# Kernel tuning notes

Hardware: AMD Instinct MI355X
Metric: run time of the kernel (lower is better)

## Reference

```python
import jax, jax.numpy as jnp
import numpy as np

B, C, H, W = 2, 128, 64, 256
G, P, EXP = 8, 4, 2
D = C // G


def _conv1x1(x, w, b):
    # x: (b,c,h,w), w: (o,c), b: (o,)
    return jnp.einsum('bchw,oc->bohw', x, w) + b[None, :, None, None]


def _lin_sample(value, x):
    # value: (b,g,d,h,w); x: (b,g,p,h,w) pixel coords along W -> (b,g,d,p,h,w)
    Bv, Gv, Dv, Hv, Wv = value.shape
    Pv = x.shape[2]
    xc = jnp.clip(x, 0.0, Wv - 1.0)
    x0 = jnp.floor(xc)
    i0 = x0.astype(jnp.int32)
    i1 = jnp.minimum(i0 + 1, Wv - 1)
    t = (xc - x0)[:, :, None]  # (b,g,1,p,h,w)
    shape = (Bv, Gv, Dv, Pv, Hv, Wv)
    v = jnp.broadcast_to(value[:, :, :, None], shape)
    v0 = jnp.take_along_axis(v, jnp.broadcast_to(i0[:, :, None], shape), axis=-1)
    v1 = jnp.take_along_axis(v, jnp.broadcast_to(i1[:, :, None], shape), axis=-1)
    return v0 * (1.0 - t) + v1 * t


def _layernorm_c(x, g, b):
    mu = jnp.mean(x, axis=1, keepdims=True)
    var = jnp.mean((x - mu) ** 2, axis=1, keepdims=True)
    return (x - mu) * jax.lax.rsqrt(var + 1e-5) * g[None, :, None, None] + b[None, :, None, None]


def _forward(ml, mr, fl, fr, nl, nr, gml, gmr, cap, gap,
             wv, bv, wn, bn, woc, boc, wog, bog, wa, ba, wo, bo,
             lw, lb, w1, b1, w2, b2):
    mask = jnp.concatenate([gml, gmr], axis=0)   # (2B,1,H,W)
    q = jnp.concatenate([ml, mr], axis=0)        # (2B,C,H,W)
    ctx = jnp.concatenate([fr, fl], axis=0)      # cross: right feats for left queries
    geo = jnp.concatenate([nr, nl], axis=0)      # (2B,3,H,W)
    B2 = q.shape[0]
    # deformable 1D cross-attention (normal-guided)
    value = _conv1x1(ctx, wv, bv).reshape(B2, G, D, H, W)
    nfeat = _conv1x1(geo, wn, bn).reshape(B2, G, D, H, W)
    off_c = _conv1x1(q, woc, boc).reshape(B2, G, P, H, W)
    off_g = _conv1x1(q, wog, bog).reshape(B2, G, P, H, W)
    attn = jax.nn.softmax(_conv1x1(q, wa, ba).reshape(B2, G, 2 * P, H, W), axis=2)
    ctx_kp = jnp.clip(cap * (W - 1.0) + off_c, 0.0, W - 1.0)
    geo_kp = jnp.clip(gap * (W - 1.0) + off_g, 0.0, W - 1.0)
    s_ctx = _lin_sample(value, ctx_kp)           # (2B,G,D,P,H,W)
    s_geo = _lin_sample(nfeat, geo_kp)
    sampled = jnp.concatenate([s_ctx, s_geo], axis=3)  # (2B,G,D,2P,H,W)
    agg = jnp.einsum('bgdphw,bgphw->bgdhw', sampled, attn).reshape(B2, C, H, W)
    upd = _conv1x1(agg, wo, bo) * mask
    # residual + LayerNorm over channels + 1x1-conv FFN
    x = q + upd
    x = _layernorm_c(x, lw, lb)
    h1 = _conv1x1(x, w1, b1)
    x = x + _conv1x1(h1 * jax.nn.sigmoid(h1), w2, b2)
    return x, ctx_kp, geo_kp


def setup_inputs() -> dict:
    key = jax.random.key(0)
    ks = jax.random.split(key, 20)
    f32 = jnp.float32
    def n(k, shape, s=1.0):
        return jax.random.normal(k, shape, dtype=f32) * s
    return {
        'match_left': n(ks[0], (B, C, H, W)),
        'match_right': n(ks[1], (B, C, H, W)),
        'feat_left': n(ks[2], (B, C, H, W)),
        'feat_right': n(ks[3], (B, C, H, W)),
        'normal_left': n(ks[4], (B, 3, H, W)),
        'normal_right': n(ks[5], (B, 3, H, W)),
        'gate_mask_left': jax.random.uniform(ks[6], (B, 1, H, W), dtype=f32),
        'gate_mask_right': jax.random.uniform(ks[7], (B, 1, H, W), dtype=f32),
        'context_anchor_points': jax.random.uniform(ks[8], (2 * B, G, P, H, W), dtype=f32),
        'geometric_anchor_points': jax.random.uniform(ks[9], (2 * B, G, P, H, W), dtype=f32),
        'w_value': n(ks[10], (C, C), 0.02), 'b_value': jnp.zeros((C,), f32),
        'w_normal': n(ks[11], (C, 3), 0.02), 'b_normal': jnp.zeros((C,), f32),
        'w_off_ctx': n(ks[12], (G * P, C), 0.02), 'b_off_ctx': jnp.zeros((G * P,), f32),
        'w_off_geo': n(ks[13], (G * P, C), 0.02), 'b_off_geo': jnp.zeros((G * P,), f32),
        'w_attn': n(ks[14], (G * 2 * P, C), 0.02), 'b_attn': jnp.zeros((G * 2 * P,), f32),
        'w_out': n(ks[15], (C, C), 0.02), 'b_out': jnp.zeros((C,), f32),
        'ln_w': jnp.ones((C,), f32), 'ln_b': jnp.zeros((C,), f32),
        'w_ff1': n(ks[16], (EXP * C, C), 0.02), 'b_ff1': jnp.zeros((EXP * C,), f32),
        'w_ff2': n(ks[17], (C, EXP * C), 0.02), 'b_ff2': jnp.zeros((C,), f32),
    }


def reference(match_left, match_right, feat_left, feat_right, normal_left, normal_right,
              gate_mask_left, gate_mask_right, context_anchor_points, geometric_anchor_points,
              w_value, b_value, w_normal, b_normal, w_off_ctx, b_off_ctx, w_off_geo, b_off_geo,
              w_attn, b_attn, w_out, b_out, ln_w, ln_b, w_ff1, b_ff1, w_ff2, b_ff2):
    x, ckp, gkp = _forward(match_left, match_right, feat_left, feat_right, normal_left, normal_right,
                           gate_mask_left, gate_mask_right, context_anchor_points, geometric_anchor_points,
                           w_value, b_value, w_normal, b_normal, w_off_ctx, b_off_ctx, w_off_geo, b_off_geo,
                           w_attn, b_attn, w_out, b_out, ln_w, ln_b, w_ff1, b_ff1, w_ff2, b_ff2)
    ml, mr = jnp.split(x, 2, axis=0)
    return (ml, mr, ckp, gkp)
```

## Files before the change

kernel.cpp:

```cpp
#include <hip/hip_runtime.h>
#include <cstdint>
#include <math.h>

#define B2v 4
#define Cc  128
#define Hh  64
#define Ww  256
#define Gg  8
#define Pp  4
#define HW  (Hh*Ww)
#define CHW (Cc*HW)

typedef float f32x4 __attribute__((ext_vector_type(4)));
typedef short s16x8 __attribute__((ext_vector_type(8)));
typedef short s16x4 __attribute__((ext_vector_type(4)));

__device__ __forceinline__ short f2bf(float x) {
    union { float f; unsigned u; } a; a.f = x;
    unsigned r = a.u + 0x7fffu + ((a.u >> 16) & 1u);
    return (short)(r >> 16);
}
__device__ __forceinline__ float bf2f(short s) {
    union { unsigned u; float f; } a; a.u = ((unsigned)(unsigned short)s) << 16;
    return a.f;
}
__device__ __forceinline__ unsigned pack2_bf(float f0, float f1) {
    union { float f; unsigned u; } a, b; a.f = f0; b.f = f1;
    return __builtin_amdgcn_perm(b.u, a.u, 0x07060302);
}

__global__ __launch_bounds__(256) void prep_kernel(
    const float* __restrict__ wv, const float* __restrict__ woc,
    const float* __restrict__ wog, const float* __restrict__ wa,
    const float* __restrict__ wo, const float* __restrict__ w1,
    const float* __restrict__ w2,
    const float* __restrict__ boc, const float* __restrict__ bog,
    const float* __restrict__ ba,
    short* __restrict__ wbf, float* __restrict__ bq)
{
    int i = blockIdx.x * 256 + threadIdx.x;
    if (i < 16384) wbf[i] = f2bf(wv[i]);
    else if (i < 32768) {
        int j = i - 16384; int r = j >> 7, c = j & 127;
        float v = (r < 32) ? woc[r * 128 + c] : (r < 64) ? wog[(r - 32) * 128 + c]
                                              : wa[(r - 64) * 128 + c];
        wbf[i] = f2bf(v);
    }
    else if (i < 49152)  wbf[i] = f2bf(wo[i - 32768]);
    else if (i < 81920)  wbf[i] = f2bf(w1[i - 49152]);
    else if (i < 114688) wbf[i] = f2bf(w2[i - 81920]);
    else if (i < 114816) {
        int r = i - 114688;
        bq[r] = (r < 32) ? boc[r] : (r < 64) ? bog[r - 32] : ba[r - 64];
    }
}

__global__ __launch_bounds__(256, 4) void kv_kernel(
    const float* __restrict__ fl, const float* __restrict__ fr,
    const short* __restrict__ wv_bf, const float* __restrict__ bv,
    short* __restrict__ value_pl)
{
    __shared__ short sB[64 * 136];
    const int t = threadIdx.x;
    const int lane = t & 63;
    const int ww = t >> 6;
    const int lm = lane & 15, lq = lane >> 4;
    const int wt = blockIdx.x, h = blockIdx.y, b = blockIdx.z;
    const int w0 = wt * 64;
    const int hWw = h * Ww;

    const float* src = (b < 2) ? fr + (size_t)b * CHW : fl + (size_t)(b - 2) * CHW;

    {
        const int c0 = ww * 32;
        const size_t rowbase = (size_t)c0 * HW + hWw + w0 + lane;
#pragma unroll
        for (int k = 0; k < 16; k++) {
            float f0 = src[rowbase + (size_t)(2 * k) * HW];
            float f1 = src[rowbase + (size_t)(2 * k + 1) * HW];
            *(unsigned*)(&sB[lane * 136 + c0 + 2 * k]) = pack2_bf(f0, f1);
        }
    }
    __syncthreads();

    f32x4 acc[2][4];
#pragma unroll
    for (int i = 0; i < 2; i++)
#pragma unroll
        for (int nt = 0; nt < 4; nt++) acc[i][nt] = (f32x4){0.f, 0.f, 0.f, 0.f};

#pragma unroll
    for (int kk = 0; kk < 4; kk++) {
        s16x8 a[2], bf[4];
#pragma unroll
        for (int i = 0; i < 2; i++)
            a[i] = *(const s16x8*)(wv_bf + (size_t)((ww * 2 + i) * 16 + lm) * 128 + kk * 32 + lq * 8);
#pragma unroll
        for (int nt = 0; nt < 4; nt++)
            bf[nt] = *(const s16x8*)(&sB[(nt * 16 + lm) * 136 + kk * 32 + lq * 8]);
#pragma unroll
        for (int i = 0; i < 2; i++)
#pragma unroll
            for (int nt = 0; nt < 4; nt++)
                acc[i][nt] = __builtin_amdgcn_mfma_f32_16x16x32_bf16(a[i], bf[nt], acc[i][nt], 0, 0, 0);
    }

#pragma unroll
    for (int i = 0; i < 2; i++) {
        const int ob = ww * 32 + i * 16 + lq * 4;
        float bias[4];
#pragma unroll
        for (int r = 0; r < 4; r++) bias[r] = bv[ob + r];
#pragma unroll
        for (int nt = 0; nt < 4; nt++) {
            const int wg = nt * 16 + lm;
#pragma unroll
            for (int r = 0; r < 4; r++)
                value_pl[(size_t)(b * Cc + ob + r) * HW + hWw + w0 + wg] =
                    f2bf(acc[i][nt][r] + bias[r]);
        }
    }
}

__global__ __launch_bounds__(256, 4) void qp_kernel(
    const float* __restrict__ mlq, const float* __restrict__ mrq,
    const short* __restrict__ wq_bf, const float* __restrict__ bq,
    const float* __restrict__ cap, const float* __restrict__ gap,
    float* __restrict__ attn_pl, float* __restrict__ ckp_out, float* __restrict__ gkp_out)
{
    __shared__ float sP[128 * 64];
    short* const sB = (short*)sP;
    const int t = threadIdx.x;
    const int lane = t & 63;
    const int ww = t >> 6;
    const int lm = lane & 15, lq = lane >> 4;
    const int wt = blockIdx.x, h = blockIdx.y, b = blockIdx.z;
    const int w0 = wt * 64;
    const int hWw = h * Ww;

    const float* src = (b < 2) ? mlq + (size_t)b * CHW : mrq + (size_t)(b - 2) * CHW;

    {
        const int c0 = ww * 32;
        const size_t rowbase = (size_t)c0 * HW + hWw + w0 + lane;
#pragma unroll
        for (int k = 0; k < 16; k++) {
            float f0 = src[rowbase + (size_t)(2 * k) * HW];
            float f1 = src[rowbase + (size_t)(2 * k + 1) * HW];
            *(unsigned*)(&sB[lane * 136 + c0 + 2 * k]) = pack2_bf(f0, f1);
        }
    }
    __syncthreads();

    f32x4 acc[2][4];
#pragma unroll
    for (int i = 0; i < 2; i++)
#pragma unroll
        for (int nt = 0; nt < 4; nt++) acc[i][nt] = (f32x4){0.f, 0.f, 0.f, 0.f};

#pragma unroll
    for (int kk = 0; kk < 4; kk++) {
        s16x8 a[2], bf[4];
#pragma unroll
        for (int i = 0; i < 2; i++)
            a[i] = *(const s16x8*)(wq_bf + (size_t)((ww * 2 + i) * 16 + lm) * 128 + kk * 32 + lq * 8);
#pragma unroll
        for (int nt = 0; nt < 4; nt++)
            bf[nt] = *(const s16x8*)(&sB[(nt * 16 + lm) * 136 + kk * 32 + lq * 8]);
#pragma unroll
        for (int i = 0; i < 2; i++)
#pragma unroll
            for (int nt = 0; nt < 4; nt++)
                acc[i][nt] = __builtin_amdgcn_mfma_f32_16x16x32_bf16(a[i], bf[nt], acc[i][nt], 0, 0, 0);
    }
    __syncthreads();

#pragma unroll
    for (int i = 0; i < 2; i++) {
        const int ob = ww * 32 + i * 16 + lq * 4;
        float bias[4];
#pragma unroll
        for (int r = 0; r < 4; r++) bias[r] = bq[ob + r];
#pragma unroll
        for (int nt = 0; nt < 4; nt++) {
            const int wg = nt * 16 + lm;
#pragma unroll
            for (int r = 0; r < 4; r++)
                sP[(ob + r) * 64 + wg] = acc[i][nt][r] + bias[r];
        }
    }
    __syncthreads();

    for (int pi = t; pi < 512; pi += 256) {
        int g = pi >> 6;
        int w = pi & 63;
        float L[8], m = -1e30f;
#pragma unroll
        for (int j = 0; j < 8; j++) { L[j] = sP[(64 + g * 8 + j) * 64 + w]; m = fmaxf(m, L[j]); }
        float s = 0.f;
#pragma unroll
        for (int j = 0; j < 8; j++) { L[j] = expf(L[j] - m); s += L[j]; }
        float inv = 1.f / s;
#pragma unroll
        for (int j = 0; j < 8; j++)
            attn_pl[((((size_t)b * Gg + g) * 8 + j) * Hh + h) * Ww + w0 + w] = L[j] * inv;
#pragma unroll
        for (int p = 0; p < 4; p++) {
            size_t kidx = ((((size_t)b * Gg + g) * Pp + p) * Hh + h) * Ww + w0 + w;
            float oc = sP[(g * 4 + p) * 64 + w];
            float og = sP[(32 + g * 4 + p) * 64 + w];
            float ck = fminf(fmaxf(cap[kidx] * 255.0f + oc, 0.f), 255.f);
            float gk = fminf(fmaxf(gap[kidx] * 255.0f + og, 0.f), 255.f);
            ckp_out[kidx] = ck;
            gkp_out[kidx] = gk;
        }
    }
}

__global__ __launch_bounds__(256) void samp_kernel(
    const short* __restrict__ value_pl,
    const float* __restrict__ nl, const float* __restrict__ nr,
    const float* __restrict__ wn, const float* __restrict__ bn,
    const float* __restrict__ attn_pl,
    const float* __restrict__ ckp, const float* __restrict__ gkp,
    short* __restrict__ agg_bf)
{
    __shared__ float vrow[Ww * 17];
    __shared__ float sgeo[3][Ww];
    __shared__ float swn[16][4];
    const int t = threadIdx.x;
    const int g = blockIdx.x, h = blockIdx.y, b = blockIdx.z;

#pragma unroll
    for (int r = 0; r < 16; r++)
        vrow[t * 17 + r] = bf2f(value_pl[(((size_t)b * Cc + g * 16 + r) * Hh + h) * Ww + t]);
    const float* geo = (b < 2) ? nr + (size_t)b * 3 * HW : nl + (size_t)(b - 2) * 3 * HW;
#pragma unroll
    for (int e = 0; e < 3; e++) sgeo[e][t] = geo[(size_t)e * HW + h * Ww + t];
    if (t < 16) {
        swn[t][0] = wn[(g * 16 + t) * 3 + 0];
        swn[t][1] = wn[(g * 16 + t) * 3 + 1];
        swn[t][2] = wn[(g * 16 + t) * 3 + 2];
        swn[t][3] = bn[g * 16 + t];
    }
    __syncthreads();

    const int w = t;
    float a8[8], kp8[8];
#pragma unroll
    for (int j = 0; j < 8; j++)
        a8[j] = attn_pl[((((size_t)b * Gg + g) * 8 + j) * Hh + h) * Ww + w];
#pragma unroll
    for (int p = 0; p < 4; p++) {
        size_t kidx = ((((size_t)b * Gg + g) * Pp + p) * Hh + h) * Ww + w;
        kp8[p]     = ckp[kidx];
        kp8[4 + p] = gkp[kidx];
    }

    float acc[16];
#pragma unroll
    for (int d = 0; d < 16; d++) acc[d] = 0.f;

#pragma unroll
    for (int j = 0; j < 4; j++) {
        float x = kp8[j];
        int i0 = (int)floorf(x);
        int i1 = min(i0 + 1, Ww - 1);
        float tt = x - (float)i0;
        float c0 = a8[j] * (1.f - tt);
        float c1 = a8[j] * tt;
#pragma unroll
        for (int d = 0; d < 16; d++)
            acc[d] += c0 * vrow[i0 * 17 + d] + c1 * vrow[i1 * 17 + d];
    }
    {
        float gs0 = 0.f, gs1 = 0.f, gs2 = 0.f, asum = 0.f;
#pragma unroll
        for (int j = 4; j < 8; j++) {
            float x = kp8[j];
            int i0 = (int)floorf(x);
            int i1 = min(i0 + 1, Ww - 1);
            float tt = x - (float)i0;
            float c0 = a8[j] * (1.f - tt);
            float c1 = a8[j] * tt;
            gs0 += c0 * sgeo[0][i0] + c1 * sgeo[0][i1];
            gs1 += c0 * sgeo[1][i0] + c1 * sgeo[1][i1];
            gs2 += c0 * sgeo[2][i0] + c1 * sgeo[2][i1];
            asum += a8[j];
        }
#pragma unroll
        for (int d = 0; d < 16; d++)
            acc[d] += swn[d][0] * gs0 + swn[d][1] * gs1 + swn[d][2] * gs2 + swn[d][3] * asum;
    }

    union { uint4 v[2]; short s[16]; } pk;
#pragma unroll
    for (int d = 0; d < 16; d++) pk.s[d] = f2bf(acc[d]);
    short* dst = agg_bf + ((size_t)((b * Hh + h) * Ww + w)) * 128 + g * 16;
    *(uint4*)(dst)     = pk.v[0];
    *(uint4*)(dst + 8) = pk.v[1];
}

__global__ __launch_bounds__(256, 3) void ffn_kernel(
    const short* __restrict__ agg_bf,
    const float* __restrict__ mlq, const float* __restrict__ mrq,
    const float* __restrict__ gml, const float* __restrict__ gmr,
    const short* __restrict__ wo_bf, const float* __restrict__ bo,
    const float* __restrict__ lnw, const float* __restrict__ lnb,
    const short* __restrict__ w1_bf, const float* __restrict__ b1,
    const short* __restrict__ w2_bf, const float* __restrict__ b2,
    float* __restrict__ out_ml, float* __restrict__ out_mr)
{
    __shared__ short sB[64 * 136];
    __shared__ short hb[64 * 136];
    __shared__ float red[2][4][64];
    __shared__ float stats[2][64];

    const int t    = threadIdx.x;
    const int lane = t & 63;
    const int ww   = t >> 6;
    const int lm   = lane & 15;
    const int lq   = lane >> 4;
    const int wt = blockIdx.x, h = blockIdx.y, b = blockIdx.z;
    const int w0 = wt * 64;
    const int hWw = h * Ww;

    const uint4* gsrc = (const uint4*)(agg_bf + ((size_t)((b * Hh + h) * Ww + w0)) * 128);
#pragma unroll
    for (int i = 0; i < 4; i++) {
        int chunk = i * 256 + t;
        int w = chunk >> 4, cc = chunk & 15;
        uint4 v = gsrc[chunk];
        *(uint4*)(&sB[w * 136 + cc * 8]) = v;
    }
    __syncthreads();

    f32x4 acc1[2][4];
#pragma unroll
    for (int i = 0; i < 2; i++)
#pragma unroll
        for (int nt = 0; nt < 4; nt++) acc1[i][nt] = (f32x4){0.f, 0.f, 0.f, 0.f};

#pragma unroll
    for (int kk = 0; kk < 4; kk++) {
        s16x8 a[2], bf[4];
#pragma unroll
        for (int i = 0; i < 2; i++)
            a[i] = *(const s16x8*)(wo_bf + (size_t)((ww * 2 + i) * 16 + lm) * 128 + kk * 32 + lq * 8);
#pragma unroll
        for (int nt = 0; nt < 4; nt++)
            bf[nt] = *(const s16x8*)(&sB[(nt * 16 + lm) * 136 + kk * 32 + lq * 8]);
#pragma unroll
        for (int i = 0; i < 2; i++)
#pragma unroll
            for (int nt = 0; nt < 4; nt++)
                acc1[i][nt] = __builtin_amdgcn_mfma_f32_16x16x32_bf16(a[i], bf[nt], acc1[i][nt], 0, 0, 0);
    }
    __syncthreads();

    const float* msk = (b < 2) ? (gml + (size_t)b * HW) : (gmr + (size_t)(b - 2) * HW);
    const float* q   = (b < 2) ? (mlq + (size_t)b * CHW) : (mrq + (size_t)(b - 2) * CHW);
    float mvals[4];
#pragma unroll
    for (int nt = 0; nt < 4; nt++) mvals[nt] = msk[hWw + w0 + nt * 16 + lm];

#pragma unroll
    for (int i = 0; i < 2; i++) {
        const int ob = ww * 32 + i * 16 + lq * 4;
        float bias[4];
#pragma unroll
        for (int r = 0; r < 4; r++) bias[r] = bo[ob + r];
#pragma unroll
        for (int nt = 0; nt < 4; nt++) {
            const int wg = nt * 16 + lm;
            s16x4 pack;
#pragma unroll
            for (int r = 0; r < 4; r++) {
                float upd = acc1[i][nt][r] + bias[r];
                float qv = q[(size_t)(ob + r) * HW + hWw + w0 + wg];
                float x = qv + upd * mvals[nt];
                pack[r] = f2bf(x);
            }
            *(s16x4*)(&sB[wg * 136 + ob]) = pack;
        }
    }
    __syncthreads();

    {
        const int quad = ww, wl = lane;
        float xv[32];
#pragma unroll
        for (int c8 = 0; c8 < 4; c8++) {
            s16x8 v = *(const s16x8*)(&sB[wl * 136 + quad * 32 + c8 * 8]);
#pragma unroll
            for (int j = 0; j < 8; j++) xv[c8 * 8 + j] = bf2f(v[j]);
        }
        float lsum = 0.f, lsq = 0.f;
#pragma unroll
        for (int k = 0; k < 32; k++) { lsum += xv[k]; lsq += xv[k] * xv[k]; }
        red[0][quad][wl] = lsum;
        red[1][quad][wl] = lsq;
        __syncthreads();
        if (t < 64) {
            float s  = red[0][0][wl] + red[0][1][wl] + red[0][2][wl] + red[0][3][wl];
            float ss = red[1][0][wl] + red[1][1][wl] + red[1][2][wl] + red[1][3][wl];
            float mu = s * (1.f / 128.f);
            float var = ss * (1.f / 128.f) - mu * mu;
            stats[0][wl] = mu;
            stats[1][wl] = rsqrtf(var + 1e-5f);
        }
        __syncthreads();
        const float mu = stats[0][wl], rstd = stats[1][wl];
#pragma unroll
        for (int c8 = 0; c8 < 4; c8++) {
            s16x8 pack;
#pragma unroll
            for (int j = 0; j < 8; j++) {
                int c = quad * 32 + c8 * 8 + j;
                float xn = (xv[c8 * 8 + j] - mu) * rstd * lnw[c] + lnb[c];
                pack[j] = f2bf(xn);
            }
            *(s16x8*)(&sB[wl * 136 + quad * 32 + c8 * 8]) = pack;
        }
    }
    __syncthreads();

    f32x4 acc3[2][4];
#pragma unroll
    for (int i = 0; i < 2; i++)
#pragma unroll
        for (int nt = 0; nt < 4; nt++) acc3[i][nt] = (f32x4){0.f, 0.f, 0.f, 0.f};

    for (int jc = 0; jc < 2; jc++) {
        f32x4 acc2[2][4];
#pragma unroll
        for (int i = 0; i < 2; i++)
#pragma unroll
            for (int nt = 0; nt < 4; nt++) acc2[i][nt] = (f32x4){0.f, 0.f, 0.f, 0.f};

#pragma unroll
        for (int kk = 0; kk < 4; kk++) {
            s16x8 a[2], bf[4];
#pragma unroll
            for (int i = 0; i < 2; i++)
                a[i] = *(const s16x8*)(w1_bf + (size_t)(jc * 128 + ww * 32 + i * 16 + lm) * 128 + kk * 32 + lq * 8);
#pragma unroll
            for (int nt = 0; nt < 4; nt++)
                bf[nt] = *(const s16x8*)(&sB[(nt * 16 + lm) * 136 + kk * 32 + lq * 8]);
#pragma unroll
            for (int i = 0; i < 2; i++)
#pragma unroll
                for (int nt = 0; nt < 4; nt++)
                    acc2[i][nt] = __builtin_amdgcn_mfma_f32_16x16x32_bf16(a[i], bf[nt], acc2[i][nt], 0, 0, 0);
        }
#pragma unroll
        for (int i = 0; i < 2; i++) {
            const int jb = ww * 32 + i * 16 + lq * 4;
            float bias[4];
#pragma unroll
            for (int r = 0; r < 4; r++) bias[r] = b1[jc * 128 + jb + r];
#pragma unroll
            for (int nt = 0; nt < 4; nt++) {
                const int wg = nt * 16 + lm;
                s16x4 pack;
#pragma unroll
                for (int r = 0; r < 4; r++) {
                    float hv = acc2[i][nt][r] + bias[r];
                    pack[r] = f2bf(hv / (1.f + expf(-hv)));
                }
                *(s16x4*)(&hb[wg * 136 + jb]) = pack;
            }
        }
        __syncthreads();

#pragma unroll
        for (int kk = 0; kk < 4; kk++) {
            s16x8 a[2], bf[4];
#pragma unroll
            for (int i = 0; i < 2; i++)
                a[i] = *(const s16x8*)(w2_bf + (size_t)((ww * 2 + i) * 16 + lm) * 256 + jc * 128 + kk * 32 + lq * 8);
#pragma unroll
            for (int nt = 0; nt < 4; nt++)
                bf[nt] = *(const s16x8*)(&hb[(nt * 16 + lm) * 136 + kk * 32 + lq * 8]);
#pragma unroll
            for (int i = 0; i < 2; i++)
#pragma unroll
                for (int nt = 0; nt < 4; nt++)
                    acc3[i][nt] = __builtin_amdgcn_mfma_f32_16x16x32_bf16(a[i], bf[nt], acc3[i][nt], 0, 0, 0);
        }
        __syncthreads();
    }

    float* outp = (b < 2) ? (out_ml + (size_t)b * CHW) : (out_mr + (size_t)(b - 2) * CHW);
#pragma unroll
    for (int i = 0; i < 2; i++) {
        const int ob = ww * 32 + i * 16 + lq * 4;
        float b2v[4];
#pragma unroll
        for (int r = 0; r < 4; r++) b2v[r] = b2[ob + r];
#pragma unroll
        for (int nt = 0; nt < 4; nt++) {
            const int wg = nt * 16 + lm;
            s16x4 xn4 = *(const s16x4*)(&sB[wg * 136 + ob]);
#pragma unroll
            for (int r = 0; r < 4; r++) {
                float y = bf2f(xn4[r]) + b2v[r] + acc3[i][nt][r];
                outp[(size_t)(ob + r) * HW + hWw + w0 + wg] = y;
            }
        }
    }
}

extern "C" void kernel_launch(void* const* d_in, const int* in_sizes, int n_in,
                              void* d_out, int out_size, void* d_ws, size_t ws_size,
                              hipStream_t stream)
{
    const float* match_l = (const float*)d_in[0];
    const float* match_r = (const float*)d_in[1];
    const float* feat_l  = (const float*)d_in[2];
    const float* feat_r  = (const float*)d_in[3];
    const float* norm_l  = (const float*)d_in[4];
    const float* norm_r  = (const float*)d_in[5];
    const float* gml     = (const float*)d_in[6];
    const float* gmr     = (const float*)d_in[7];
    const float* cap     = (const float*)d_in[8];
    const float* gap     = (const float*)d_in[9];
    const float* wv  = (const float*)d_in[10]; const float* bv  = (const float*)d_in[11];
    const float* wn  = (const float*)d_in[12]; const float* bn  = (const float*)d_in[13];
    const float* woc = (const float*)d_in[14]; const float* boc = (const float*)d_in[15];
    const float* wog = (const float*)d_in[16]; const float* bog = (const float*)d_in[17];
    const float* wa  = (const float*)d_in[18]; const float* ba  = (const float*)d_in[19];
    const float* wo  = (const float*)d_in[20]; const float* bo  = (const float*)d_in[21];
    const float* lnw = (const float*)d_in[22]; const float* lnb = (const float*)d_in[23];
    const float* w1  = (const float*)d_in[24]; const float* b1  = (const float*)d_in[25];
    const float* w2  = (const float*)d_in[26]; const float* b2  = (const float*)d_in[27];

    float* out = (float*)d_out;
    float* out_ml  = out;
    float* out_mr  = out + (size_t)2 * CHW;
    float* ckp_out = out + (size_t)4 * CHW;
    float* gkp_out = ckp_out + (size_t)B2v * Gg * Pp * HW;

    float* ws = (float*)d_ws;
    float* attn_pl  = ws;
    float* bq       = attn_pl + (size_t)B2v * 64 * HW;
    short* value_pl = (short*)(bq + 128);
    short* agg_bf   = value_pl + (size_t)B2v * Cc * HW;
    short* wbf      = agg_bf   + (size_t)B2v * HW * Cc;
    short* wv_bf = wbf;
    short* wq_bf = wbf + 16384;
    short* wo_bf = wbf + 32768;
    short* w1_bf = wbf + 49152;
    short* w2_bf = wbf + 81920;

    dim3 blk(256);
    prep_kernel<<<dim3(449), blk, 0, stream>>>(
        wv, woc, wog, wa, wo, w1, w2, boc, bog, ba, wbf, bq);
    kv_kernel<<<dim3(4, Hh, B2v), blk, 0, stream>>>(
        feat_l, feat_r, wv_bf, bv, value_pl);
    qp_kernel<<<dim3(4, Hh, B2v), blk, 0, stream>>>(
        match_l, match_r, wq_bf, bq, cap, gap, attn_pl, ckp_out, gkp_out);
    samp_kernel<<<dim3(Gg, Hh, B2v), blk, 0, stream>>>(
        value_pl, norm_l, norm_r, wn, bn, attn_pl, ckp_out, gkp_out, agg_bf);
    ffn_kernel<<<dim3(4, Hh, B2v), blk, 0, stream>>>(
        agg_bf, match_l, match_r, gml, gmr, wo_bf, bo, lnw, lnb,
        w1_bf, b1, w2_bf, b2, out_ml, out_mr);
}
```

Before: 250.9 us.

## Fuse value, query projection, sampling and FFN into one per-row mega kernel

```diff
diff --git a/kernel.cpp b/kernel.cpp
--- a/kernel.cpp
+++ b/kernel.cpp
@@ -10,6 +10,7 @@
 #define Pp  4
 #define HW  (Hh*Ww)
 #define CHW (Cc*HW)
+#define PIT 136
 
 typedef float f32x4 __attribute__((ext_vector_type(4)));
 typedef short s16x8 __attribute__((ext_vector_type(8)));
@@ -55,458 +56,356 @@
     }
 }
 
-__global__ __launch_bounds__(256, 4) void kv_kernel(
-    const float* __restrict__ fl, const float* __restrict__ fr,
-    const short* __restrict__ wv_bf, const float* __restrict__ bv,
-    short* __restrict__ value_pl)
+__global__ __launch_bounds__(512, 2) void mega_kernel(
+    const float* __restrict__ mlq, const float* __restrict__ mrq,
+    const float* __restrict__ fl,  const float* __restrict__ fr,
+    const float* __restrict__ nl,  const float* __restrict__ nr,
+    const float* __restrict__ gml, const float* __restrict__ gmr,
+    const float* __restrict__ cap, const float* __restrict__ gap,
+    const short* __restrict__ wbf, const float* __restrict__ bq,
+    const float* __restrict__ bv,
+    const float* __restrict__ wn,  const float* __restrict__ bn,
+    const float* __restrict__ bo,
+    const float* __restrict__ lnw, const float* __restrict__ lnb,
+    const float* __restrict__ b1,  const float* __restrict__ b2,
+    float* __restrict__ out_ml, float* __restrict__ out_mr,
+    float* __restrict__ ckp_out, float* __restrict__ gkp_out)
 {
-    __shared__ short sB[64 * 136];
-    const int t = threadIdx.x;
-    const int lane = t & 63;
-    const int ww = t >> 6;
-    const int lm = lane & 15, lq = lane >> 4;
-    const int wt = blockIdx.x, h = blockIdx.y, b = blockIdx.z;
-    const int w0 = wt * 64;
-    const int hWw = h * Ww;
-
-    const float* src = (b < 2) ? fr + (size_t)b * CHW : fl + (size_t)(b - 2) * CHW;
-
-    {
-        const int c0 = ww * 32;
-        const size_t rowbase = (size_t)c0 * HW + hWw + w0 + lane;
-#pragma unroll
-        for (int k = 0; k < 16; k++) {
-            float f0 = src[rowbase + (size_t)(2 * k) * HW];
-            float f1 = src[rowbase + (size_t)(2 * k + 1) * HW];
-            *(unsigned*)(&sB[lane * 136 + c0 + 2 * k]) = pack2_bf(f0, f1);
-        }
-    }
-    __syncthreads();
-
-    f32x4 acc[2][4];
-#pragma unroll
-    for (int i = 0; i < 2; i++)
-#pragma unroll
-        for (int nt = 0; nt < 4; nt++) acc[i][nt] = (f32x4){0.f, 0.f, 0.f, 0.f};
-
-#pragma unroll
-    for (int kk = 0; kk < 4; kk++) {
-        s16x8 a[2], bf[4];
-#pragma unroll
-        for (int i = 0; i < 2; i++)
-            a[i] = *(const s16x8*)(wv_bf + (size_t)((ww * 2 + i) * 16 + lm) * 128 + kk * 32 + lq * 8);
-#pragma unroll
-        for (int nt = 0; nt < 4; nt++)
-            bf[nt] = *(const s16x8*)(&sB[(nt * 16 + lm) * 136 + kk * 32 + lq * 8]);
-#pragma unroll
-        for (int i = 0; i < 2; i++)
-#pragma unroll
-            for (int nt = 0; nt < 4; nt++)
-                acc[i][nt] = __builtin_amdgcn_mfma_f32_16x16x32_bf16(a[i], bf[nt], acc[i][nt], 0, 0, 0);
-    }
-
-#pragma unroll
-    for (int i = 0; i < 2; i++) {
-        const int ob = ww * 32 + i * 16 + lq * 4;
-        float bias[4];
-#pragma unroll
-        for (int r = 0; r < 4; r++) bias[r] = bv[ob + r];
-#pragma unroll
-        for (int nt = 0; nt < 4; nt++) {
-            const int wg = nt * 16 + lm;
-#pragma unroll
-            for (int r = 0; r < 4; r++)
-                value_pl[(size_t)(b * Cc + ob + r) * HW + hWw + w0 + wg] =
-                    f2bf(acc[i][nt][r] + bias[r]);
-        }
-    }
-}
-
-__global__ __launch_bounds__(256, 4) void qp_kernel(
-    const float* __restrict__ mlq, const float* __restrict__ mrq,
-    const short* __restrict__ wq_bf, const float* __restrict__ bq,
-    const float* __restrict__ cap, const float* __restrict__ gap,
-    float* __restrict__ attn_pl, float* __restrict__ ckp_out, float* __restrict__ gkp_out)
-{
-    __shared__ float sP[128 * 64];
-    short* const sB = (short*)sP;
-    const int t = threadIdx.x;
-    const int lane = t & 63;
-    const int ww = t >> 6;
-    const int lm = lane & 15, lq = lane >> 4;
-    const int wt = blockIdx.x, h = blockIdx.y, b = blockIdx.z;
-    const int w0 = wt * 64;
-    const int hWw = h * Ww;
-
-    const float* src = (b < 2) ? mlq + (size_t)b * CHW : mrq + (size_t)(b - 2) * CHW;
-
-    {
-        const int c0 = ww * 32;
-        const size_t rowbase = (size_t)c0 * HW + hWw + w0 + lane;
-#pragma unroll
-        for (int k = 0; k < 16; k++) {
-            float f0 = src[rowbase + (size_t)(2 * k) * HW];
-            float f1 = src[rowbase + (size_t)(2 * k + 1) * HW];
-            *(unsigned*)(&sB[lane * 136 + c0 + 2 * k]) = pack2_bf(f0, f1);
-        }
-    }
-    __syncthreads();
-
-    f32x4 acc[2][4];
-#pragma unroll
-    for (int i = 0; i < 2; i++)
-#pragma unroll
-        for (int nt = 0; nt < 4; nt++) acc[i][nt] = (f32x4){0.f, 0.f, 0.f, 0.f};
-
-#pragma unroll
-    for (int kk = 0; kk < 4; kk++) {
-        s16x8 a[2], bf[4];
-#pragma unroll
-        for (int i = 0; i < 2; i++)
-            a[i] = *(const s16x8*)(wq_bf + (size_t)((ww * 2 + i) * 16 + lm) * 128 + kk * 32 + lq * 8);
-#pragma unroll
-        for (int nt = 0; nt < 4; nt++)
-            bf[nt] = *(const s16x8*)(&sB[(nt * 16 + lm) * 136 + kk * 32 + lq * 8]);
-#pragma unroll
-        for (int i = 0; i < 2; i++)
-#pragma unroll
-            for (int nt = 0; nt < 4; nt++)
-                acc[i][nt] = __builtin_amdgcn_mfma_f32_16x16x32_bf16(a[i], bf[nt], acc[i][nt], 0, 0, 0);
-    }
-    __syncthreads();
-
-#pragma unroll
-    for (int i = 0; i < 2; i++) {
-        const int ob = ww * 32 + i * 16 + lq * 4;
-        float bias[4];
-#pragma unroll
-        for (int r = 0; r < 4; r++) bias[r] = bq[ob + r];
-#pragma unroll
-        for (int nt = 0; nt < 4; nt++) {
-            const int wg = nt * 16 + lm;
-#pragma unroll
-            for (int r = 0; r < 4; r++)
-                sP[(ob + r) * 64 + wg] = acc[i][nt][r] + bias[r];
-        }
-    }
-    __syncthreads();
-
-    for (int pi = t; pi < 512; pi += 256) {
-        int g = pi >> 6;
-        int w = pi & 63;
-        float L[8], m = -1e30f;
-#pragma unroll
-        for (int j = 0; j < 8; j++) { L[j] = sP[(64 + g * 8 + j) * 64 + w]; m = fmaxf(m, L[j]); }
-        float s = 0.f;
-#pragma unroll
-        for (int j = 0; j < 8; j++) { L[j] = expf(L[j] - m); s += L[j]; }
-        float inv = 1.f / s;
-#pragma unroll
-        for (int j = 0; j < 8; j++)
-            attn_pl[((((size_t)b * Gg + g) * 8 + j) * Hh + h) * Ww + w0 + w] = L[j] * inv;
-#pragma unroll
-        for (int p = 0; p < 4; p++) {
-            size_t kidx = ((((size_t)b * Gg + g) * Pp + p) * Hh + h) * Ww + w0 + w;
-            float oc = sP[(g * 4 + p) * 64 + w];
-            float og = sP[(32 + g * 4 + p) * 64 + w];
-            float ck = fminf(fmaxf(cap[kidx] * 255.0f + oc, 0.f), 255.f);
-            float gk = fminf(fmaxf(gap[kidx] * 255.0f + og, 0.f), 255.f);
-            ckp_out[kidx] = ck;
-            gkp_out[kidx] = gk;
-        }
-    }
-}
-
-__global__ __launch_bounds__(256) void samp_kernel(
-    const short* __restrict__ value_pl,
-    const float* __restrict__ nl, const float* __restrict__ nr,
-    const float* __restrict__ wn, const float* __restrict__ bn,
-    const float* __restrict__ attn_pl,
-    const float* __restrict__ ckp, const float* __restrict__ gkp,
-    short* __restrict__ agg_bf)
-{
-    __shared__ float vrow[Ww * 17];
-    __shared__ float sgeo[3][Ww];
-    __shared__ float swn[16][4];
-    const int t = threadIdx.x;
-    const int g = blockIdx.x, h = blockIdx.y, b = blockIdx.z;
-
-#pragma unroll
-    for (int r = 0; r < 16; r++)
-        vrow[t * 17 + r] = bf2f(value_pl[(((size_t)b * Cc + g * 16 + r) * Hh + h) * Ww + t]);
-    const float* geo = (b < 2) ? nr + (size_t)b * 3 * HW : nl + (size_t)(b - 2) * 3 * HW;
-#pragma unroll
-    for (int e = 0; e < 3; e++) sgeo[e][t] = geo[(size_t)e * HW + h * Ww + t];
-    if (t < 16) {
-        swn[t][0] = wn[(g * 16 + t) * 3 + 0];
-        swn[t][1] = wn[(g * 16 + t) * 3 + 1];
-        swn[t][2] = wn[(g * 16 + t) * 3 + 2];
-        swn[t][3] = bn[g * 16 + t];
-    }
-    __syncthreads();
-
-    const int w = t;
-    float a8[8], kp8[8];
-#pragma unroll
-    for (int j = 0; j < 8; j++)
-        a8[j] = attn_pl[((((size_t)b * Gg + g) * 8 + j) * Hh + h) * Ww + w];
-#pragma unroll
-    for (int p = 0; p < 4; p++) {
-        size_t kidx = ((((size_t)b * Gg + g) * Pp + p) * Hh + h) * Ww + w;
-        kp8[p]     = ckp[kidx];
-        kp8[4 + p] = gkp[kidx];
-    }
-
-    float acc[16];
-#pragma unroll
-    for (int d = 0; d < 16; d++) acc[d] = 0.f;
-
-#pragma unroll
-    for (int j = 0; j < 4; j++) {
-        float x = kp8[j];
-        int i0 = (int)floorf(x);
-        int i1 = min(i0 + 1, Ww - 1);
-        float tt = x - (float)i0;
-        float c0 = a8[j] * (1.f - tt);
-        float c1 = a8[j] * tt;
-#pragma unroll
-        for (int d = 0; d < 16; d++)
-            acc[d] += c0 * vrow[i0 * 17 + d] + c1 * vrow[i1 * 17 + d];
-    }
-    {
-        float gs0 = 0.f, gs1 = 0.f, gs2 = 0.f, asum = 0.f;
-#pragma unroll
-        for (int j = 4; j < 8; j++) {
-            float x = kp8[j];
-            int i0 = (int)floorf(x);
-            int i1 = min(i0 + 1, Ww - 1);
-            float tt = x - (float)i0;
-            float c0 = a8[j] * (1.f - tt);
-            float c1 = a8[j] * tt;
-            gs0 += c0 * sgeo[0][i0] + c1 * sgeo[0][i1];
-            gs1 += c0 * sgeo[1][i0] + c1 * sgeo[1][i1];
-            gs2 += c0 * sgeo[2][i0] + c1 * sgeo[2][i1];
-            asum += a8[j];
-        }
-#pragma unroll
-        for (int d = 0; d < 16; d++)
-            acc[d] += swn[d][0] * gs0 + swn[d][1] * gs1 + swn[d][2] * gs2 + swn[d][3] * asum;
-    }
-
-    union { uint4 v[2]; short s[16]; } pk;
-#pragma unroll
-    for (int d = 0; d < 16; d++) pk.s[d] = f2bf(acc[d]);
-    short* dst = agg_bf + ((size_t)((b * Hh + h) * Ww + w)) * 128 + g * 16;
-    *(uint4*)(dst)     = pk.v[0];
-    *(uint4*)(dst + 8) = pk.v[1];
-}
-
-__global__ __launch_bounds__(256, 3) void ffn_kernel(
-    const short* __restrict__ agg_bf,
-    const float* __restrict__ mlq, const float* __restrict__ mrq,
-    const float* __restrict__ gml, const float* __restrict__ gmr,
-    const short* __restrict__ wo_bf, const float* __restrict__ bo,
-    const float* __restrict__ lnw, const float* __restrict__ lnb,
-    const short* __restrict__ w1_bf, const float* __restrict__ b1,
-    const short* __restrict__ w2_bf, const float* __restrict__ b2,
-    float* __restrict__ out_ml, float* __restrict__ out_mr)
-{
-    __shared__ short sB[64 * 136];
-    __shared__ short hb[64 * 136];
-    __shared__ float red[2][4][64];
-    __shared__ float stats[2][64];
+    __shared__ short buf1[256 * PIT];
+    __shared__ short buf2[256 * PIT];
+    __shared__ float sgeo[3 * 256];
+    __shared__ float swn4[128 * 4];
+    __shared__ float redS[512], redQ[512];
+    __shared__ float smu[256], srs[256];
+
+    const short* wv_bf = wbf;
+    const short* wq_bf = wbf + 16384;
+    const short* wo_bf = wbf + 32768;
+    const short* w1_bf = wbf + 49152;
+    const short* w2_bf = wbf + 81920;
 
     const int t    = threadIdx.x;
     const int lane = t & 63;
     const int ww   = t >> 6;
     const int lm   = lane & 15;
     const int lq   = lane >> 4;
-    const int wt = blockIdx.x, h = blockIdx.y, b = blockIdx.z;
-    const int w0 = wt * 64;
+    const int h = blockIdx.x, b = blockIdx.y;
     const int hWw = h * Ww;
-
-    const uint4* gsrc = (const uint4*)(agg_bf + ((size_t)((b * Hh + h) * Ww + w0)) * 128);
-#pragma unroll
-    for (int i = 0; i < 4; i++) {
-        int chunk = i * 256 + t;
-        int w = chunk >> 4, cc = chunk & 15;
-        uint4 v = gsrc[chunk];
-        *(uint4*)(&sB[w * 136 + cc * 8]) = v;
-    }
-    __syncthreads();
-
-    f32x4 acc1[2][4];
-#pragma unroll
-    for (int i = 0; i < 2; i++)
-#pragma unroll
-        for (int nt = 0; nt < 4; nt++) acc1[i][nt] = (f32x4){0.f, 0.f, 0.f, 0.f};
-
-#pragma unroll
-    for (int kk = 0; kk < 4; kk++) {
-        s16x8 a[2], bf[4];
-#pragma unroll
-        for (int i = 0; i < 2; i++)
-            a[i] = *(const s16x8*)(wo_bf + (size_t)((ww * 2 + i) * 16 + lm) * 128 + kk * 32 + lq * 8);
-#pragma unroll
-        for (int nt = 0; nt < 4; nt++)
-            bf[nt] = *(const s16x8*)(&sB[(nt * 16 + lm) * 136 + kk * 32 + lq * 8]);
-#pragma unroll
-        for (int i = 0; i < 2; i++)
-#pragma unroll
-            for (int nt = 0; nt < 4; nt++)
-                acc1[i][nt] = __builtin_amdgcn_mfma_f32_16x16x32_bf16(a[i], bf[nt], acc1[i][nt], 0, 0, 0);
-    }
-    __syncthreads();
-
-    const float* msk = (b < 2) ? (gml + (size_t)b * HW) : (gmr + (size_t)(b - 2) * HW);
-    const float* q   = (b < 2) ? (mlq + (size_t)b * CHW) : (mrq + (size_t)(b - 2) * CHW);
-    float mvals[4];
-#pragma unroll
-    for (int nt = 0; nt < 4; nt++) mvals[nt] = msk[hWw + w0 + nt * 16 + lm];
-
-#pragma unroll
-    for (int i = 0; i < 2; i++) {
-        const int ob = ww * 32 + i * 16 + lq * 4;
+    const int px   = t & 255;
+    const int half = t >> 8;
+
+    const float* ctx = (b < 2) ? fr + (size_t)b * CHW : fl + (size_t)(b - 2) * CHW;
+    const float* q   = (b < 2) ? mlq + (size_t)b * CHW : mrq + (size_t)(b - 2) * CHW;
+    const float* geo = (b < 2) ? nr + (size_t)b * 3 * HW : nl + (size_t)(b - 2) * 3 * HW;
+    const float* msk = (b < 2) ? gml + (size_t)b * HW : gmr + (size_t)(b - 2) * HW;
+    float* outp = (b < 2) ? out_ml + (size_t)b * CHW : out_mr + (size_t)(b - 2) * CHW;
+
+    for (int i = t; i < 768; i += 512) sgeo[i] = geo[(size_t)(i >> 8) * HW + hWw + (i & 255)];
+    if (t < 128) {
+        swn4[t * 4 + 0] = wn[t * 3 + 0];
+        swn4[t * 4 + 1] = wn[t * 3 + 1];
+        swn4[t * 4 + 2] = wn[t * 3 + 2];
+        swn4[t * 4 + 3] = bn[t];
+    }
+
+    {
+        const int c0 = ww * 16;
+#pragma unroll
+        for (int sub = 0; sub < 4; sub++) {
+            const int p = sub * 64 + lane;
+            const size_t base = (size_t)c0 * HW + hWw + p;
+#pragma unroll
+            for (int k = 0; k < 8; k++) {
+                float f0 = ctx[base + (size_t)(2 * k) * HW];
+                float f1 = ctx[base + (size_t)(2 * k + 1) * HW];
+                *(unsigned*)(&buf1[p * PIT + c0 + 2 * k]) = pack2_bf(f0, f1);
+            }
+        }
+    }
+    __syncthreads();
+
+    {
+        f32x4 acc[16];
+#pragma unroll
+        for (int nt = 0; nt < 16; nt++) acc[nt] = (f32x4){0.f, 0.f, 0.f, 0.f};
+#pragma unroll
+        for (int kk = 0; kk < 4; kk++) {
+            s16x8 a = *(const s16x8*)(wv_bf + (size_t)(ww * 16 + lm) * 128 + kk * 32 + lq * 8);
+#pragma unroll
+            for (int nt = 0; nt < 16; nt++) {
+                s16x8 bfv = *(const s16x8*)(&buf1[(nt * 16 + lm) * PIT + kk * 32 + lq * 8]);
+                acc[nt] = __builtin_amdgcn_mfma_f32_16x16x32_bf16(a, bfv, acc[nt], 0, 0, 0);
+            }
+        }
+        const int ob = ww * 16 + lq * 4;
         float bias[4];
 #pragma unroll
+        for (int r = 0; r < 4; r++) bias[r] = bv[ob + r];
+#pragma unroll
+        for (int nt = 0; nt < 16; nt++) {
+            const int wg = nt * 16 + lm;
+            s16x4 pk;
+#pragma unroll
+            for (int r = 0; r < 4; r++) pk[r] = f2bf(acc[nt][r] + bias[r]);
+            *(s16x4*)(&buf2[wg * PIT + ob]) = pk;
+        }
+    }
+    __syncthreads();
+
+    {
+        const int c0 = ww * 16;
+#pragma unroll
+        for (int sub = 0; sub < 4; sub++) {
+            const int p = sub * 64 + lane;
+            const size_t base = (size_t)c0 * HW + hWw + p;
+#pragma unroll
+            for (int k = 0; k < 8; k++) {
+                float f0 = q[base + (size_t)(2 * k) * HW];
+                float f1 = q[base + (size_t)(2 * k + 1) * HW];
+                *(unsigned*)(&buf1[p * PIT + c0 + 2 * k]) = pack2_bf(f0, f1);
+            }
+        }
+    }
+    __syncthreads();
+
+    {
+        f32x4 acc[16];
+#pragma unroll
+        for (int nt = 0; nt < 16; nt++) acc[nt] = (f32x4){0.f, 0.f, 0.f, 0.f};
+#pragma unroll
+        for (int kk = 0; kk < 4; kk++) {
+            s16x8 a = *(const s16x8*)(wq_bf + (size_t)(ww * 16 + lm) * 128 + kk * 32 + lq * 8);
+#pragma unroll
+            for (int nt = 0; nt < 16; nt++) {
+                s16x8 bfv = *(const s16x8*)(&buf1[(nt * 16 + lm) * PIT + kk * 32 + lq * 8]);
+                acc[nt] = __builtin_amdgcn_mfma_f32_16x16x32_bf16(a, bfv, acc[nt], 0, 0, 0);
+            }
+        }
+        __syncthreads();
+        const int ob = ww * 16 + lq * 4;
+        float bias[4];
+#pragma unroll
+        for (int r = 0; r < 4; r++) bias[r] = bq[ob + r];
+#pragma unroll
+        for (int nt = 0; nt < 16; nt++) {
+            const int wg = nt * 16 + lm;
+            s16x4 pk;
+#pragma unroll
+            for (int r = 0; r < 4; r++) pk[r] = f2bf(acc[nt][r] + bias[r]);
+            *(s16x4*)(&buf1[wg * PIT + ob]) = pk;
+        }
+    }
+    __syncthreads();
+
+    float attnr[4][8], kpr[4][8];
+#pragma unroll
+    for (int gi = 0; gi < 4; gi++) {
+        const int g = half * 4 + gi;
+        s16x8 lg = *(const s16x8*)(&buf1[px * PIT + 64 + g * 8]);
+        float L[8], m = -1e30f;
+#pragma unroll
+        for (int j = 0; j < 8; j++) { L[j] = bf2f(lg[j]); m = fmaxf(m, L[j]); }
+        float s = 0.f;
+#pragma unroll
+        for (int j = 0; j < 8; j++) { L[j] = expf(L[j] - m); s += L[j]; }
+        float inv = 1.f / s;
+#pragma unroll
+        for (int j = 0; j < 8; j++) attnr[gi][j] = L[j] * inv;
+#pragma unroll
+        for (int p = 0; p < 4; p++) {
+            size_t kidx = ((((size_t)b * Gg + g) * Pp + p) * Hh + h) * Ww + px;
+            float oc = bf2f(buf1[px * PIT + g * 4 + p]);
+            float og = bf2f(buf1[px * PIT + 32 + g * 4 + p]);
+            float ck = fminf(fmaxf(cap[kidx] * 255.0f + oc, 0.f), 255.f);
+            float gk = fminf(fmaxf(gap[kidx] * 255.0f + og, 0.f), 255.f);
+            ckp_out[kidx] = ck;
+            gkp_out[kidx] = gk;
+            kpr[gi][p] = ck;
+            kpr[gi][4 + p] = gk;
+        }
+    }
+    __syncthreads();
+
+#pragma unroll
+    for (int gi = 0; gi < 4; gi++) {
+        const int g = half * 4 + gi;
+        float a16[16];
+#pragma unroll
+        for (int d = 0; d < 16; d++) a16[d] = 0.f;
+#pragma unroll
+        for (int j = 0; j < 4; j++) {
+            float x = kpr[gi][j];
+            int i0 = (int)floorf(x);
+            int i1 = min(i0 + 1, Ww - 1);
+            float tt = x - (float)i0;
+            float c0 = attnr[gi][j] * (1.f - tt);
+            float c1 = attnr[gi][j] * tt;
+            s16x8 v0a = *(const s16x8*)(&buf2[i0 * PIT + g * 16]);
+            s16x8 v0b = *(const s16x8*)(&buf2[i0 * PIT + g * 16 + 8]);
+            s16x8 v1a = *(const s16x8*)(&buf2[i1 * PIT + g * 16]);
+            s16x8 v1b = *(const s16x8*)(&buf2[i1 * PIT + g * 16 + 8]);
+#pragma unroll
+            for (int d = 0; d < 8; d++) {
+                a16[d]     += c0 * bf2f(v0a[d]) + c1 * bf2f(v1a[d]);
+                a16[8 + d] += c0 * bf2f(v0b[d]) + c1 * bf2f(v1b[d]);
+            }
+        }
+        {
+            float gs0 = 0.f, gs1 = 0.f, gs2 = 0.f, as = 0.f;
+#pragma unroll
+            for (int j = 4; j < 8; j++) {
+                float x = kpr[gi][j];
+                int i0 = (int)floorf(x);
+                int i1 = min(i0 + 1, Ww - 1);
+                float tt = x - (float)i0;
+                float c0 = attnr[gi][j] * (1.f - tt);
+                float c1 = attnr[gi][j] * tt;
+                gs0 += c0 * sgeo[i0] + c1 * sgeo[i1];
+                gs1 += c0 * sgeo[256 + i0] + c1 * sgeo[256 + i1];
+                gs2 += c0 * sgeo[512 + i0] + c1 * sgeo[512 + i1];
+                as  += attnr[gi][j];
+            }
+#pragma unroll
+            for (int d = 0; d < 16; d++) {
+                const float* w4 = &swn4[(g * 16 + d) * 4];
+                a16[d] += w4[0] * gs0 + w4[1] * gs1 + w4[2] * gs2 + w4[3] * as;
+            }
+        }
+        s16x8 p0, p1;
+#pragma unroll
+        for (int d = 0; d < 8; d++) { p0[d] = f2bf(a16[d]); p1[d] = f2bf(a16[8 + d]); }
+        *(s16x8*)(&buf1[px * PIT + g * 16])     = p0;
+        *(s16x8*)(&buf1[px * PIT + g * 16 + 8]) = p1;
+    }
+    __syncthreads();
+
+    {
+        f32x4 acc1[16];
+#pragma unroll
+        for (int nt = 0; nt < 16; nt++) acc1[nt] = (f32x4){0.f, 0.f, 0.f, 0.f};
+#pragma unroll
+        for (int kk = 0; kk < 4; kk++) {
+            s16x8 a = *(const s16x8*)(wo_bf + (size_t)(ww * 16 + lm) * 128 + kk * 32 + lq * 8);
+#pragma unroll
+            for (int nt = 0; nt < 16; nt++) {
+                s16x8 bfv = *(const s16x8*)(&buf1[(nt * 16 + lm) * PIT + kk * 32 + lq * 8]);
+                acc1[nt] = __builtin_amdgcn_mfma_f32_16x16x32_bf16(a, bfv, acc1[nt], 0, 0, 0);
+            }
+        }
+        __syncthreads();
+        const int ob = ww * 16 + lq * 4;
+        float bias[4];
+#pragma unroll
         for (int r = 0; r < 4; r++) bias[r] = bo[ob + r];
 #pragma unroll
-        for (int nt = 0; nt < 4; nt++) {
+        for (int nt = 0; nt < 16; nt++) {
             const int wg = nt * 16 + lm;
-            s16x4 pack;
+            float mval = msk[hWw + wg];
+            s16x4 pk;
 #pragma unroll
             for (int r = 0; r < 4; r++) {
-                float upd = acc1[i][nt][r] + bias[r];
-                float qv = q[(size_t)(ob + r) * HW + hWw + w0 + wg];
-                float x = qv + upd * mvals[nt];
-                pack[r] = f2bf(x);
-            }
-            *(s16x4*)(&sB[wg * 136 + ob]) = pack;
-        }
-    }
-    __syncthreads();
-
-    {
-        const int quad = ww, wl = lane;
-        float xv[32];
-#pragma unroll
-        for (int c8 = 0; c8 < 4; c8++) {
-            s16x8 v = *(const s16x8*)(&sB[wl * 136 + quad * 32 + c8 * 8]);
-#pragma unroll
-            for (int j = 0; j < 8; j++) xv[c8 * 8 + j] = bf2f(v[j]);
-        }
-        float lsum = 0.f, lsq = 0.f;
-#pragma unroll
-        for (int k = 0; k < 32; k++) { lsum += xv[k]; lsq += xv[k] * xv[k]; }
-        red[0][quad][wl] = lsum;
-        red[1][quad][wl] = lsq;
-        __syncthreads();
-        if (t < 64) {
-            float s  = red[0][0][wl] + red[0][1][wl] + red[0][2][wl] + red[0][3][wl];
-            float ss = red[1][0][wl] + red[1][1][wl] + red[1][2][wl] + red[1][3][wl];
+                float upd = acc1[nt][r] + bias[r];
+                float qv = q[(size_t)(ob + r) * HW + hWw + wg];
+                pk[r] = f2bf(qv + upd * mval);
+            }
+            *(s16x4*)(&buf1[wg * PIT + ob]) = pk;
+        }
+    }
+    __syncthreads();
+
+    {
+        float ls = 0.f, lsq = 0.f;
+#pragma unroll
+        for (int c8 = 0; c8 < 8; c8++) {
+            s16x8 v = *(const s16x8*)(&buf1[px * PIT + half * 64 + c8 * 8]);
+#pragma unroll
+            for (int j = 0; j < 8; j++) { float f = bf2f(v[j]); ls += f; lsq += f * f; }
+        }
+        redS[t] = ls; redQ[t] = lsq;
+        __syncthreads();
+        if (t < 256) {
+            float s  = redS[t] + redS[t + 256];
+            float qq = redQ[t] + redQ[t + 256];
             float mu = s * (1.f / 128.f);
-            float var = ss * (1.f / 128.f) - mu * mu;
-            stats[0][wl] = mu;
-            stats[1][wl] = rsqrtf(var + 1e-5f);
-        }
-        __syncthreads();
-        const float mu = stats[0][wl], rstd = stats[1][wl];
-#pragma unroll
-        for (int c8 = 0; c8 < 4; c8++) {
-            s16x8 pack;
+            float var = qq * (1.f / 128.f) - mu * mu;
+            smu[t] = mu;
+            srs[t] = rsqrtf(var + 1e-5f);
+        }
+        __syncthreads();
+        const float mu = smu[px], rs = srs[px];
+#pragma unroll
+        for (int c8 = 0; c8 < 8; c8++) {
+            s16x8 v = *(const s16x8*)(&buf1[px * PIT + half * 64 + c8 * 8]);
+            s16x8 pk;
 #pragma unroll
             for (int j = 0; j < 8; j++) {
-                int c = quad * 32 + c8 * 8 + j;
-                float xn = (xv[c8 * 8 + j] - mu) * rstd * lnw[c] + lnb[c];
-                pack[j] = f2bf(xn);
-            }
-            *(s16x8*)(&sB[wl * 136 + quad * 32 + c8 * 8]) = pack;
-        }
-    }
-    __syncthreads();
-
-    f32x4 acc3[2][4];
-#pragma unroll
-    for (int i = 0; i < 2; i++)
-#pragma unroll
-        for (int nt = 0; nt < 4; nt++) acc3[i][nt] = (f32x4){0.f, 0.f, 0.f, 0.f};
+                int c = half * 64 + c8 * 8 + j;
+                pk[j] = f2bf((bf2f(v[j]) - mu) * rs * lnw[c] + lnb[c]);
+            }
+            *(s16x8*)(&buf1[px * PIT + half * 64 + c8 * 8]) = pk;
+        }
+    }
+    __syncthreads();
+
+    f32x4 acc3[16];
+#pragma unroll
+    for (int nt = 0; nt < 16; nt++) acc3[nt] = (f32x4){0.f, 0.f, 0.f, 0.f};
 
     for (int jc = 0; jc < 2; jc++) {
-        f32x4 acc2[2][4];
-#pragma unroll
-        for (int i = 0; i < 2; i++)
-#pragma unroll
-            for (int nt = 0; nt < 4; nt++) acc2[i][nt] = (f32x4){0.f, 0.f, 0.f, 0.f};
-
+        f32x4 acc2[16];
+#pragma unroll
+        for (int nt = 0; nt < 16; nt++) acc2[nt] = (f32x4){0.f, 0.f, 0.f, 0.f};
 #pragma unroll
         for (int kk = 0; kk < 4; kk++) {
-            s16x8 a[2], bf[4];
-#pragma unroll
-            for (int i = 0; i < 2; i++)
-                a[i] = *(const s16x8*)(w1_bf + (size_t)(jc * 128 + ww * 32 + i * 16 + lm) * 128 + kk * 32 + lq * 8);
-#pragma unroll
-            for (int nt = 0; nt < 4; nt++)
-                bf[nt] = *(const s16x8*)(&sB[(nt * 16 + lm) * 136 + kk * 32 + lq * 8]);
-#pragma unroll
-            for (int i = 0; i < 2; i++)
-#pragma unroll
-                for (int nt = 0; nt < 4; nt++)
-                    acc2[i][nt] = __builtin_amdgcn_mfma_f32_16x16x32_bf16(a[i], bf[nt], acc2[i][nt], 0, 0, 0);
-        }
-#pragma unroll
-        for (int i = 0; i < 2; i++) {
-            const int jb = ww * 32 + i * 16 + lq * 4;
+            s16x8 a = *(const s16x8*)(w1_bf + (size_t)(jc * 128 + ww * 16 + lm) * 128 + kk * 32 + lq * 8);
+#pragma unroll
+            for (int nt = 0; nt < 16; nt++) {
+                s16x8 bfv = *(const s16x8*)(&buf1[(nt * 16 + lm) * PIT + kk * 32 + lq * 8]);
+                acc2[nt] = __builtin_amdgcn_mfma_f32_16x16x32_bf16(a, bfv, acc2[nt], 0, 0, 0);
+            }
+        }
+        {
+            const int jb = ww * 16 + lq * 4;
             float bias[4];
 #pragma unroll
             for (int r = 0; r < 4; r++) bias[r] = b1[jc * 128 + jb + r];
 #pragma unroll
-            for (int nt = 0; nt < 4; nt++) {
+            for (int nt = 0; nt < 16; nt++) {
                 const int wg = nt * 16 + lm;
-                s16x4 pack;
+                s16x4 pk;
 #pragma unroll
                 for (int r = 0; r < 4; r++) {
-                    float hv = acc2[i][nt][r] + bias[r];
-                    pack[r] = f2bf(hv / (1.f + expf(-hv)));
+                    float hv = acc2[nt][r] + bias[r];
+                    pk[r] = f2bf(hv / (1.f + expf(-hv)));
                 }
-                *(s16x4*)(&hb[wg * 136 + jb]) = pack;
-            }
-        }
-        __syncthreads();
-
+                *(s16x4*)(&buf2[wg * PIT + jb]) = pk;
+            }
+        }
+        __syncthreads();
 #pragma unroll
         for (int kk = 0; kk < 4; kk++) {
-            s16x8 a[2], bf[4];
-#pragma unroll
-            for (int i = 0; i < 2; i++)
-                a[i] = *(const s16x8*)(w2_bf + (size_t)((ww * 2 + i) * 16 + lm) * 256 + jc * 128 + kk * 32 + lq * 8);
-#pragma unroll
-            for (int nt = 0; nt < 4; nt++)
-                bf[nt] = *(const s16x8*)(&hb[(nt * 16 + lm) * 136 + kk * 32 + lq * 8]);
-#pragma unroll
-            for (int i = 0; i < 2; i++)
-#pragma unroll
-                for (int nt = 0; nt < 4; nt++)
-                    acc3[i][nt] = __builtin_amdgcn_mfma_f32_16x16x32_bf16(a[i], bf[nt], acc3[i][nt], 0, 0, 0);
-        }
-        __syncthreads();
-    }
-
-    float* outp = (b < 2) ? (out_ml + (size_t)b * CHW) : (out_mr + (size_t)(b - 2) * CHW);
-#pragma unroll
-    for (int i = 0; i < 2; i++) {
-        const int ob = ww * 32 + i * 16 + lq * 4;
+            s16x8 a = *(const s16x8*)(w2_bf + (size_t)(ww * 16 + lm) * 256 + jc * 128 + kk * 32 + lq * 8);
+#pragma unroll
+            for (int nt = 0; nt < 16; nt++) {
+                s16x8 bfv = *(const s16x8*)(&buf2[(nt * 16 + lm) * PIT + kk * 32 + lq * 8]);
+                acc3[nt] = __builtin_amdgcn_mfma_f32_16x16x32_bf16(a, bfv, acc3[nt], 0, 0, 0);
+            }
+        }
+        __syncthreads();
+    }
+
+    {
+        const int ob = ww * 16 + lq * 4;
         float b2v[4];
 #pragma unroll
         for (int r = 0; r < 4; r++) b2v[r] = b2[ob + r];
 #pragma unroll
-        for (int nt = 0; nt < 4; nt++) {
+        for (int nt = 0; nt < 16; nt++) {
             const int wg = nt * 16 + lm;
-            s16x4 xn4 = *(const s16x4*)(&sB[wg * 136 + ob]);
-#pragma unroll
-            for (int r = 0; r < 4; r++) {
-                float y = bf2f(xn4[r]) + b2v[r] + acc3[i][nt][r];
-                outp[(size_t)(ob + r) * HW + hWw + w0 + wg] = y;
-            }
+            s16x4 xn4 = *(const s16x4*)(&buf1[wg * PIT + ob]);
+#pragma unroll
+            for (int r = 0; r < 4; r++)
+                outp[(size_t)(ob + r) * HW + hWw + wg] = bf2f(xn4[r]) + b2v[r] + acc3[nt][r];
         }
     }
 }
@@ -542,27 +441,13 @@
     float* gkp_out = ckp_out + (size_t)B2v * Gg * Pp * HW;
 
     float* ws = (float*)d_ws;
-    float* attn_pl  = ws;
-    float* bq       = attn_pl + (size_t)B2v * 64 * HW;
-    short* value_pl = (short*)(bq + 128);
-    short* agg_bf   = value_pl + (size_t)B2v * Cc * HW;
-    short* wbf      = agg_bf   + (size_t)B2v * HW * Cc;
-    short* wv_bf = wbf;
-    short* wq_bf = wbf + 16384;
-    short* wo_bf = wbf + 32768;
-    short* w1_bf = wbf + 49152;
-    short* w2_bf = wbf + 81920;
-
-    dim3 blk(256);
-    prep_kernel<<<dim3(449), blk, 0, stream>>>(
+    float* bq  = ws;
+    short* wbf = (short*)(bq + 128);
+
+    prep_kernel<<<dim3(449), dim3(256), 0, stream>>>(
         wv, woc, wog, wa, wo, w1, w2, boc, bog, ba, wbf, bq);
-    kv_kernel<<<dim3(4, Hh, B2v), blk, 0, stream>>>(
-        feat_l, feat_r, wv_bf, bv, value_pl);
-    qp_kernel<<<dim3(4, Hh, B2v), blk, 0, stream>>>(
-        match_l, match_r, wq_bf, bq, cap, gap, attn_pl, ckp_out, gkp_out);
-    samp_kernel<<<dim3(Gg, Hh, B2v), blk, 0, stream>>>(
-        value_pl, norm_l, norm_r, wn, bn, attn_pl, ckp_out, gkp_out, agg_bf);
-    ffn_kernel<<<dim3(4, Hh, B2v), blk, 0, stream>>>(
-        agg_bf, match_l, match_r, gml, gmr, wo_bf, bo, lnw, lnb,
-        w1_bf, b1, w2_bf, b2, out_ml, out_mr);
-}
+    mega_kernel<<<dim3(Hh, B2v), dim3(512), 0, stream>>>(
+        match_l, match_r, feat_l, feat_r, norm_l, norm_r, gml, gmr, cap, gap,
+        wbf, bq, bv, wn, bn, bo, lnw, lnb, b1, b2,
+        out_ml, out_mr, ckp_out, gkp_out);
+}
```

Result: faster. 222.3 us (-11.4%).
